# Kernel tuning notes

Hardware: AMD Instinct MI355X
Metric: run time of the kernel (lower is better)

The kernel has to match this reference:

```python
import jax, jax.numpy as jnp
import numpy as np


def _cdist(a, b):
    # a: [B,J,D], b: [B,P,D] -> Euclidean distances [B,J,P]
    # matmul-based expansion, matching torch.cdist(p=2) default path
    a2 = jnp.sum(a * a, axis=-1)          # [B,J]
    b2 = jnp.sum(b * b, axis=-1)          # [B,P]
    ab = jnp.einsum('bjd,bpd->bjp', a, b)  # [B,J,P]
    sq = a2[:, :, None] + b2[:, None, :] - 2.0 * ab
    return jnp.sqrt(jnp.maximum(sq, 0.0))


def setup_inputs() -> dict:
    key = jax.random.key(0)
    k1, k2, k3 = jax.random.split(key, 3)
    B, J, P, D = 64, 42, 16384, 3
    pred_joints = jax.random.normal(k1, (B, J, D), dtype=jnp.float32)
    object_points = jax.random.normal(k2, (B, P, D), dtype=jnp.float32)
    gt_distance = jax.random.uniform(k3, (B, J), dtype=jnp.float32)
    return {"pred_joints": pred_joints, "object_points": object_points,
            "gt_distance": gt_distance}


def reference(pred_joints, object_points, gt_distance):
    pred_dist = _cdist(pred_joints, object_points)   # [B,J,P]
    min_val = jnp.min(pred_dist, axis=2)             # [B,J]
    return jnp.mean((min_val - gt_distance) ** 2)    # scalar MSE
```

## Files before the change

### kernel.cpp

```cpp
#include <hip/hip_runtime.h>
#include <math.h>

#define B   64
#define NJ  42
#define NP  16384
#define CHUNKS 8
#define PC  (NP / CHUNKS)
#define TPB 256
#define PPT (PC / TPB)
#define NPAIR (PPT / 2)
#define RSTRIDE 260

typedef float v2f __attribute__((ext_vector_type(2)));

__global__ __launch_bounds__(TPB) void sdl_min_kernel(
    const float* __restrict__ joints,
    const float* __restrict__ pts,
    float* __restrict__ part)
{
    __shared__ __align__(16) float4 sj[NJ];
    __shared__ __align__(16) float  red[NJ * RSTRIDE];

    const int tid = threadIdx.x;
    const int b   = blockIdx.x >> 3;
    const int ch  = blockIdx.x & 7;

    if (tid < NJ) {
        const float* jp = joints + (b * NJ + tid) * 3;
        float x = jp[0], y = jp[1], z = jp[2];
        sj[tid] = make_float4(x, y, z, fmaf(x, x, fmaf(y, y, z * z)));
    }

    v2f npx[NPAIR], npy[NPAIR], npz[NPAIR], q[NPAIR];
    const float* pb = pts + (size_t)(b * NP + ch * PC) * 3;
#pragma unroll
    for (int k = 0; k < NPAIR; ++k) {
        int i0 = ((2 * k)     * TPB + tid) * 3;
        int i1 = ((2 * k + 1) * TPB + tid) * 3;
        float x0 = pb[i0], y0 = pb[i0 + 1], z0 = pb[i0 + 2];
        float x1 = pb[i1], y1 = pb[i1 + 1], z1 = pb[i1 + 2];
        npx[k] = (v2f){-x0, -x1};
        npy[k] = (v2f){-y0, -y1};
        npz[k] = (v2f){-z0, -z1};
        q[k]   = (v2f){0.5f * fmaf(x0, x0, fmaf(y0, y0, z0 * z0)),
                       0.5f * fmaf(x1, x1, fmaf(y1, y1, z1 * z1))};
    }
    __syncthreads();

    float m[NJ];
#pragma unroll
    for (int j = 0; j < NJ; ++j) m[j] = 3.0e38f;

#pragma unroll
    for (int j = 0; j < NJ; ++j) {
        float4 Jv = sj[j];
        v2f jx = (v2f){Jv.x, Jv.x};
        v2f jy = (v2f){Jv.y, Jv.y};
        v2f jz = (v2f){Jv.z, Jv.z};
        float mj = m[j];
#pragma unroll
        for (int k = 0; k < NPAIR; ++k) {
            v2f t = npz[k] * jz + q[k];
            t     = npy[k] * jy + t;
            t     = npx[k] * jx + t;
            mj = fminf(fminf(mj, t.x), t.y);
        }
        m[j] = mj;
    }

#pragma unroll
    for (int j = 0; j < NJ; ++j) red[j * RSTRIDE + tid] = m[j];
    __syncthreads();

    if (tid < NJ) {
        const float4* row = (const float4*)(red + tid * RSTRIDE);
        float4 a = row[0];
        for (int i = 1; i < TPB / 4; ++i) {
            float4 v = row[i];
            a.x = fminf(a.x, v.x); a.y = fminf(a.y, v.y);
            a.z = fminf(a.z, v.z); a.w = fminf(a.w, v.w);
        }
        float mn = fminf(fminf(a.x, a.y), fminf(a.z, a.w));
        float d2 = fmaxf(fmaf(2.0f, mn, sj[tid].w), 0.0f);
        part[ch * (B * NJ) + b * NJ + tid] = d2;
    }
}

__global__ __launch_bounds__(1024) void sdl_final_kernel(
    const float* __restrict__ part,
    const float* __restrict__ gt,
    float* __restrict__ out)
{
    const int tid = threadIdx.x;
    float acc = 0.0f;
    for (int i = tid; i < B * NJ; i += 1024) {
        float mn = part[i];
#pragma unroll
        for (int c = 1; c < CHUNKS; ++c) mn = fminf(mn, part[c * (B * NJ) + i]);
        float diff = sqrtf(mn) - gt[i];
        acc = fmaf(diff, diff, acc);
    }
#pragma unroll
    for (int off = 32; off > 0; off >>= 1)
        acc += __shfl_xor(acc, off);
    __shared__ float wsum[16];
    if ((tid & 63) == 0) wsum[tid >> 6] = acc;
    __syncthreads();
    if (tid == 0) {
        float s = 0.0f;
#pragma unroll
        for (int w = 0; w < 16; ++w) s += wsum[w];
        out[0] = s * (1.0f / (B * NJ));
    }
}

extern "C" void kernel_launch(void* const* d_in, const int* in_sizes, int n_in,
                              void* d_out, int out_size, void* d_ws, size_t ws_size,
                              hipStream_t stream) {
    const float* pred = (const float*)d_in[0];
    const float* obj  = (const float*)d_in[1];
    const float* gt   = (const float*)d_in[2];
    float* part = (float*)d_ws;

    sdl_min_kernel<<<B * CHUNKS, TPB, 0, stream>>>(pred, obj, part);
    sdl_final_kernel<<<1, 1024, 0, stream>>>(part, gt, (float*)d_out);
}
```

Measured before the change: 73.12 us.

## Fuse final MSE reduction into min kernel via last-block atomic counter

Merges the two-kernel pipeline into a single launch. Each block publishes its partial minima, fences, and atomically increments a workspace counter. The block that arrives last performs the cross-chunk min, sqrt and MSE reduction, then resets the counter. This removes a second kernel launch and its dependency gap, at the cost of fences, an atomic per block, and reliance on the workspace counter's initial state (it accepts either zero or an 0xAA fill pattern).

Measured after the change: 91.21 us. +24.7%, slower.

```diff
diff --git a/kernel.cpp b/kernel.cpp
--- a/kernel.cpp
+++ b/kernel.cpp
@@ -10,16 +10,21 @@
 #define PPT (PC / TPB)
 #define NPAIR (PPT / 2)
 #define RSTRIDE 260
+#define NBLK (B * CHUNKS)
 
 typedef float v2f __attribute__((ext_vector_type(2)));
 
-__global__ __launch_bounds__(TPB) void sdl_min_kernel(
+__global__ __launch_bounds__(TPB) void sdl_fused_kernel(
     const float* __restrict__ joints,
     const float* __restrict__ pts,
-    float* __restrict__ part)
+    const float* __restrict__ gt,
+    float* __restrict__ part,
+    unsigned int* __restrict__ counter,
+    float* __restrict__ out)
 {
     __shared__ __align__(16) float4 sj[NJ];
     __shared__ __align__(16) float  red[NJ * RSTRIDE];
+    __shared__ int is_last;
 
     const int tid = threadIdx.x;
     const int b   = blockIdx.x >> 3;
@@ -83,34 +88,37 @@
         float mn = fminf(fminf(a.x, a.y), fminf(a.z, a.w));
         float d2 = fmaxf(fmaf(2.0f, mn, sj[tid].w), 0.0f);
         part[ch * (B * NJ) + b * NJ + tid] = d2;
+        __threadfence();
     }
-}
+    __syncthreads();
 
-__global__ __launch_bounds__(1024) void sdl_final_kernel(
-    const float* __restrict__ part,
-    const float* __restrict__ gt,
-    float* __restrict__ out)
-{
-    const int tid = threadIdx.x;
-    float acc = 0.0f;
-    for (int i = tid; i < B * NJ; i += 1024) {
-        float mn = part[i];
+    if (tid == 0) {
+        unsigned int old = __hip_atomic_fetch_add(counter, 1u,
+                              __ATOMIC_ACQ_REL, __HIP_MEMORY_SCOPE_AGENT);
+        is_last = (old == (NBLK - 1u)) || (old == 0xAAAAAAAAu + (NBLK - 1u));
+    }
+    __syncthreads();
+
+    if (is_last) {
+        __threadfence();
+        float acc = 0.0f;
+        for (int i = tid; i < B * NJ; i += TPB) {
+            float mn = part[i];
 #pragma unroll
-        for (int c = 1; c < CHUNKS; ++c) mn = fminf(mn, part[c * (B * NJ) + i]);
-        float diff = sqrtf(mn) - gt[i];
-        acc = fmaf(diff, diff, acc);
-    }
+            for (int c = 1; c < CHUNKS; ++c) mn = fminf(mn, part[c * (B * NJ) + i]);
+            float diff = sqrtf(mn) - gt[i];
+            acc = fmaf(diff, diff, acc);
+        }
 #pragma unroll
-    for (int off = 32; off > 0; off >>= 1)
-        acc += __shfl_xor(acc, off);
-    __shared__ float wsum[16];
-    if ((tid & 63) == 0) wsum[tid >> 6] = acc;
-    __syncthreads();
-    if (tid == 0) {
-        float s = 0.0f;
-#pragma unroll
-        for (int w = 0; w < 16; ++w) s += wsum[w];
-        out[0] = s * (1.0f / (B * NJ));
+        for (int off = 32; off > 0; off >>= 1)
+            acc += __shfl_xor(acc, off);
+        if ((tid & 63) == 0) red[tid >> 6] = acc;
+        __syncthreads();
+        if (tid == 0) {
+            out[0] = (red[0] + red[1] + red[2] + red[3]) * (1.0f / (B * NJ));
+            __hip_atomic_fetch_add(counter, (unsigned int)(0u - NBLK),
+                                   __ATOMIC_RELAXED, __HIP_MEMORY_SCOPE_AGENT);
+        }
     }
 }
 
@@ -121,7 +129,8 @@
     const float* obj  = (const float*)d_in[1];
     const float* gt   = (const float*)d_in[2];
     float* part = (float*)d_ws;
+    unsigned int* counter = (unsigned int*)d_ws + CHUNKS * B * NJ;
 
-    sdl_min_kernel<<<B * CHUNKS, TPB, 0, stream>>>(pred, obj, part);
-    sdl_final_kernel<<<1, 1024, 0, stream>>>(part, gt, (float*)d_out);
+    sdl_fused_kernel<<<NBLK, TPB, 0, stream>>>(pred, obj, gt, part, counter,
+                                               (float*)d_out);
 }
```
